# Kernel optimization log

Hardware: AMD Instinct MI355X
Metric: run time of the kernel (lower is better)

Reference implementation:

```python
import jax, jax.numpy as jnp
import numpy as np

FP8_MAX = 448.0  # e4m3 max
SCALE_MARGIN = 0.8


def _fp8_quant_dequant(t, scale):
    # scaled value is <= 448*0.8 by construction, so no saturation/overflow
    q = (t / scale).astype(jnp.float8_e4m3fn)
    return q.astype(jnp.float32) * scale


def setup_inputs() -> dict:
    key = jax.random.key(0)
    k1, k2 = jax.random.split(key)
    B, S, D_IN, D_OUT = 4, 2048, 2048, 2048
    x = jax.random.normal(k1, (B, S, D_IN), dtype=jnp.float32)
    weight = jax.random.normal(k2, (D_OUT, D_IN), dtype=jnp.float32)
    bias = jnp.zeros((D_OUT,), dtype=jnp.float32)
    return {"x": x, "weight": weight, "bias": bias}


def reference(x, weight, bias):
    # Shared FP8ScalingManager: amax history = [amax_x] for x, then [amax_x, amax_w] for w.
    amax_x = jnp.max(jnp.abs(x))
    amax_w = jnp.max(jnp.abs(weight))
    x_scale = amax_x / (FP8_MAX * SCALE_MARGIN)
    w_scale = jnp.maximum(amax_x, amax_w) / (FP8_MAX * SCALE_MARGIN)  # history max
    x_scale = jax.lax.stop_gradient(x_scale)  # .item() detaches in torch
    w_scale = jax.lax.stop_gradient(w_scale)
    # quantize to fp8 e4m3, dequantize, scaled matmul (math of torch._scaled_mm)
    x_dq = _fp8_quant_dequant(x, x_scale)      # [B,S,Din]
    w_dq = _fp8_quant_dequant(weight, w_scale)  # [Dout,Din]
    out = jnp.einsum('bsd,od->bso', x_dq, w_dq)  # [B,S,Dout]
    return out + bias
```

## Files before the change

### kernel.cpp

```cpp
#include <hip/hip_runtime.h>
#include <stdint.h>

typedef float v4f __attribute__((ext_vector_type(4)));
typedef int v8i __attribute__((ext_vector_type(8)));

#define FP8_DENOM 358.4f


__device__ __forceinline__ unsigned pack4_fp8(float a, float b, float c, float d) {
  int v = 0;
  v = __builtin_amdgcn_cvt_pk_fp8_f32(a, b, v, false);
  v = __builtin_amdgcn_cvt_pk_fp8_f32(c, d, v, true);
  return (unsigned)v;
}

__device__ __forceinline__ void gload_lds16(const void* g, void* l) {
  __builtin_amdgcn_global_load_lds(
      (const __attribute__((address_space(1))) uint32_t*)(uintptr_t)g,
      (__attribute__((address_space(3))) uint32_t*)(uint32_t)(uintptr_t)l,
      16, 0, 0);
}


__global__ void __launch_bounds__(256) amax_part(const float4* __restrict__ x,
                                                 const float4* __restrict__ w,
                                                 unsigned* __restrict__ amax) {
  const int b = blockIdx.x, t = threadIdx.x;
  const float4* p = (b < 1024) ? x : w;
  const long base = (long)((b < 1024) ? b : (b - 1024)) * 4096;
  float m0 = 0.f, m1 = 0.f, m2 = 0.f, m3 = 0.f;
#pragma unroll
  for (int j = 0; j < 4; ++j) {
    float4 v0 = p[base + (j * 4 + 0) * 256 + t];
    float4 v1 = p[base + (j * 4 + 1) * 256 + t];
    float4 v2 = p[base + (j * 4 + 2) * 256 + t];
    float4 v3 = p[base + (j * 4 + 3) * 256 + t];
    m0 = fmaxf(m0, fmaxf(fmaxf(fabsf(v0.x), fabsf(v0.y)), fmaxf(fabsf(v0.z), fabsf(v0.w))));
    m1 = fmaxf(m1, fmaxf(fmaxf(fabsf(v1.x), fabsf(v1.y)), fmaxf(fabsf(v1.z), fabsf(v1.w))));
    m2 = fmaxf(m2, fmaxf(fmaxf(fabsf(v2.x), fabsf(v2.y)), fmaxf(fabsf(v2.z), fabsf(v2.w))));
    m3 = fmaxf(m3, fmaxf(fmaxf(fabsf(v3.x), fabsf(v3.y)), fmaxf(fabsf(v3.z), fabsf(v3.w))));
  }
  float m = fmaxf(fmaxf(m0, m1), fmaxf(m2, m3));
#pragma unroll
  for (int off = 32; off > 0; off >>= 1)
    m = fmaxf(m, __shfl_down(m, off, 64));
  __shared__ float red[4];
  const int lane = t & 63, wvid = t >> 6;
  if (lane == 0) red[wvid] = m;
  __syncthreads();
  if (t == 0)
    atomicMax(amax + ((b < 1024) ? 0 : 1),
              __float_as_uint(fmaxf(fmaxf(red[0], red[1]), fmaxf(red[2], red[3]))));
}


__global__ void __launch_bounds__(256) quant2_kernel(
    const float4* __restrict__ x, unsigned* __restrict__ xq,
    const float4* __restrict__ w, unsigned* __restrict__ wq,
    const unsigned* __restrict__ amax) {
  const int t = threadIdx.x;
  const int isw = ((int)blockIdx.x >= 4096) ? 1 : 0;
  const float ax = __uint_as_float(amax[0]);
  const float aw = __uint_as_float(amax[1]);
  const float s = (isw ? fmaxf(ax, aw) : ax) / FP8_DENOM;
  const float rs = 1.0f / s;
  const float4* in = isw ? w : x;
  unsigned* outq = isw ? wq : xq;
  const long base = (long)(isw ? ((int)blockIdx.x - 4096) : (int)blockIdx.x) * 1024;
#pragma unroll
  for (int j = 0; j < 4; ++j) {
    float4 v = in[base + j * 256 + t];
    outq[base + j * 256 + t] = pack4_fp8(v.x * rs, v.y * rs, v.z * rs, v.w * rs);
  }
}


__global__ void __launch_bounds__(512, 2) gemm_mx(
    const uint8_t* __restrict__ Aq, const uint8_t* __restrict__ Bq,
    const float* __restrict__ bias, float* __restrict__ out,
    const unsigned* __restrict__ amax) {
  constexpr int K = 2048, N = 2048, BK = 128, ITERS = K / BK;
  __shared__ alignas(16) uint8_t sA[2][256 * BK];
  __shared__ alignas(16) uint8_t sB[2][256 * BK];

  const int tid = threadIdx.x;
  const int lane = tid & 63;
  const int wid = tid >> 6;
  const int wy = wid >> 2, wx = wid & 3;
  const long tileM = (long)blockIdx.y * 256;
  const long tileN = (long)blockIdx.x * 256;

  v4f acc[8][4];
#pragma unroll
  for (int i = 0; i < 8; ++i)
#pragma unroll
    for (int j = 0; j < 4; ++j) acc[i][j] = (v4f)(0.f);

  const int srow = tid >> 3;
  const int schunk = (tid & 7) ^ (srow & 7);
  const uint8_t* gA = Aq + (tileM + srow) * K + schunk * 16;
  const uint8_t* gB = Bq + (tileN + srow) * K + schunk * 16;

  const int q = lane >> 4;
  const int mrow = lane & 15;
  const int sw = mrow & 7;
  const int aoff0 = (wy * 128 + mrow) * BK + 16 * ((2 * q) ^ sw);
  const int aoff1 = (wy * 128 + mrow) * BK + 16 * ((2 * q + 1) ^ sw);
  const int boff0 = (wx * 64 + mrow) * BK + 16 * ((2 * q) ^ sw);
  const int boff1 = (wx * 64 + mrow) * BK + 16 * ((2 * q + 1) ^ sw);

  auto stage = [&](int buf, int k0) {
#pragma unroll
    for (int s = 0; s < 4; ++s) {
      gload_lds16(gA + (long)s * 64 * K + k0, &sA[buf][s * 8192 + tid * 16]);
      gload_lds16(gB + (long)s * 64 * K + k0, &sB[buf][s * 8192 + tid * 16]);
    }
  };

  stage(0, 0);
  for (int it = 0; it < ITERS; ++it) {
    __syncthreads();
    if (it + 1 < ITERS) stage((it + 1) & 1, (it + 1) * BK);

    const uint8_t* bufA = sA[it & 1];
    const uint8_t* bufB = sB[it & 1];
    union Frag { v8i v; uint4 h[2]; };
    Frag b[4];
#pragma unroll
    for (int j = 0; j < 4; ++j) {
      b[j].h[0] = *(const uint4*)(bufB + boff0 + j * 16 * BK);
      b[j].h[1] = *(const uint4*)(bufB + boff1 + j * 16 * BK);
    }
    __builtin_amdgcn_s_setprio(1);
#pragma unroll
    for (int i = 0; i < 8; ++i) {
      Frag a;
      a.h[0] = *(const uint4*)(bufA + aoff0 + i * 16 * BK);
      a.h[1] = *(const uint4*)(bufA + aoff1 + i * 16 * BK);
#pragma unroll
      for (int j = 0; j < 4; ++j)
        acc[i][j] = __builtin_amdgcn_mfma_scale_f32_16x16x128_f8f6f4(
            a.v, b[j].v, acc[i][j],  0,  0,
             0, 0x7F7F7F7F,  0, 0x7F7F7F7F);
    }
    __builtin_amdgcn_s_setprio(0);
  }

  const float ax = __uint_as_float(amax[0]);
  const float aw = __uint_as_float(amax[1]);
  const float scale = (ax / FP8_DENOM) * (fmaxf(ax, aw) / FP8_DENOM);
#pragma unroll
  for (int j = 0; j < 4; ++j) {
    const long col = tileN + wx * 64 + j * 16 + mrow;
    const float bv = bias[col];
#pragma unroll
    for (int i = 0; i < 8; ++i) {
      const long row = tileM + wy * 128 + i * 16 + q * 4;
#pragma unroll
      for (int r = 0; r < 4; ++r)
        out[(row + r) * N + col] = acc[i][j][r] * scale + bv;
    }
  }
}


extern "C" void kernel_launch(void* const* d_in, const int* in_sizes, int n_in,
                              void* d_out, int out_size, void* d_ws, size_t ws_size,
                              hipStream_t stream) {
  const float* x = (const float*)d_in[0];
  const float* w = (const float*)d_in[1];
  const float* bias = (const float*)d_in[2];
  float* out = (float*)d_out;

  const int M = 8192, N = 2048, K = 2048;
  const long nx = (long)M * K;

  unsigned* amax = (unsigned*)d_ws;
  uint8_t* xq = (uint8_t*)d_ws + 8192;
  uint8_t* wq = xq + nx;

  hipMemsetAsync(amax, 0, 8, stream);
  amax_part<<<1280, 256, 0, stream>>>((const float4*)x, (const float4*)w, amax);
  quant2_kernel<<<5120, 256, 0, stream>>>((const float4*)x, (unsigned*)xq,
                                          (const float4*)w, (unsigned*)wq, amax);
  gemm_mx<<<dim3(N / 256, M / 256), 512, 0, stream>>>(xq, wq, bias, out, amax);
}
```

Baseline: 177.7 us.

## Prefetch two K-tiles ahead in GEMM and split amax into smaller blocks

```diff
diff --git a/kernel.cpp b/kernel.cpp
--- a/kernel.cpp
+++ b/kernel.cpp
@@ -26,21 +26,17 @@
                                                  const float4* __restrict__ w,
                                                  unsigned* __restrict__ amax) {
   const int b = blockIdx.x, t = threadIdx.x;
-  const float4* p = (b < 1024) ? x : w;
-  const long base = (long)((b < 1024) ? b : (b - 1024)) * 4096;
-  float m0 = 0.f, m1 = 0.f, m2 = 0.f, m3 = 0.f;
+  const int isw = (b >= 2048) ? 1 : 0;
+  const float4* p = isw ? w : x;
+  const long base = (long)(isw ? (b - 2048) : b) * 2048;
+  float4 v[8];
 #pragma unroll
-  for (int j = 0; j < 4; ++j) {
-    float4 v0 = p[base + (j * 4 + 0) * 256 + t];
-    float4 v1 = p[base + (j * 4 + 1) * 256 + t];
-    float4 v2 = p[base + (j * 4 + 2) * 256 + t];
-    float4 v3 = p[base + (j * 4 + 3) * 256 + t];
-    m0 = fmaxf(m0, fmaxf(fmaxf(fabsf(v0.x), fabsf(v0.y)), fmaxf(fabsf(v0.z), fabsf(v0.w))));
-    m1 = fmaxf(m1, fmaxf(fmaxf(fabsf(v1.x), fabsf(v1.y)), fmaxf(fabsf(v1.z), fabsf(v1.w))));
-    m2 = fmaxf(m2, fmaxf(fmaxf(fabsf(v2.x), fabsf(v2.y)), fmaxf(fabsf(v2.z), fabsf(v2.w))));
-    m3 = fmaxf(m3, fmaxf(fmaxf(fabsf(v3.x), fabsf(v3.y)), fmaxf(fabsf(v3.z), fabsf(v3.w))));
-  }
-  float m = fmaxf(fmaxf(m0, m1), fmaxf(m2, m3));
+  for (int j = 0; j < 8; ++j) v[j] = p[base + j * 256 + t];
+  float m = 0.f;
+#pragma unroll
+  for (int j = 0; j < 8; ++j)
+    m = fmaxf(m, fmaxf(fmaxf(fabsf(v[j].x), fabsf(v[j].y)),
+                       fmaxf(fabsf(v[j].z), fabsf(v[j].w))));
 #pragma unroll
   for (int off = 32; off > 0; off >>= 1)
     m = fmaxf(m, __shfl_down(m, off, 64));
@@ -49,7 +45,7 @@
   if (lane == 0) red[wvid] = m;
   __syncthreads();
   if (t == 0)
-    atomicMax(amax + ((b < 1024) ? 0 : 1),
+    atomicMax(amax + isw,
               __float_as_uint(fmaxf(fmaxf(red[0], red[1]), fmaxf(red[2], red[3]))));
 }
 
@@ -118,9 +114,15 @@
   };
 
   stage(0, 0);
+  stage(1, BK);
+
   for (int it = 0; it < ITERS; ++it) {
-    __syncthreads();
-    if (it + 1 < ITERS) stage((it + 1) & 1, (it + 1) * BK);
+    if (it == ITERS - 1)
+      asm volatile("s_waitcnt vmcnt(0)" ::: "memory");
+    else
+      asm volatile("s_waitcnt vmcnt(8)" ::: "memory");
+    __builtin_amdgcn_s_barrier();
+    __builtin_amdgcn_sched_barrier(0);
 
     const uint8_t* bufA = sA[it & 1];
     const uint8_t* bufB = sB[it & 1];
@@ -144,6 +146,11 @@
              0, 0x7F7F7F7F,  0, 0x7F7F7F7F);
     }
     __builtin_amdgcn_s_setprio(0);
+
+    __builtin_amdgcn_sched_barrier(0);
+    asm volatile("s_waitcnt lgkmcnt(0)" ::: "memory");
+    __builtin_amdgcn_s_barrier();
+    if (it + 2 < ITERS) stage(it & 1, (it + 2) * BK);
   }
 
   const float ax = __uint_as_float(amax[0]);
@@ -180,7 +187,7 @@
   uint8_t* wq = xq + nx;
 
   hipMemsetAsync(amax, 0, 8, stream);
-  amax_part<<<1280, 256, 0, stream>>>((const float4*)x, (const float4*)w, amax);
+  amax_part<<<2560, 256, 0, stream>>>((const float4*)x, (const float4*)w, amax);
   quant2_kernel<<<5120, 256, 0, stream>>>((const float4*)x, (unsigned*)xq,
                                           (const float4*)w, (unsigned*)wq, amax);
   gemm_mx<<<dim3(N / 256, M / 256), 512, 0, stream>>>(xq, wq, bias, out, amax);
```

After: 193.2 us. +8.7%, slower.

## Split GEMM main loop into phased barriers with staggered A/B prefetch and XCD tile remap

Applied to the files above, without the earlier changes.

```diff
diff --git a/kernel.cpp b/kernel.cpp
--- a/kernel.cpp
+++ b/kernel.cpp
@@ -26,8 +26,9 @@
                                                  const float4* __restrict__ w,
                                                  unsigned* __restrict__ amax) {
   const int b = blockIdx.x, t = threadIdx.x;
-  const float4* p = (b < 1024) ? x : w;
-  const long base = (long)((b < 1024) ? b : (b - 1024)) * 4096;
+  const int isw = (b >= 1024) ? 1 : 0;
+  const float4* p = isw ? w : x;
+  const long base = (long)(isw ? (b - 1024) : b) * 4096;
   float m0 = 0.f, m1 = 0.f, m2 = 0.f, m3 = 0.f;
 #pragma unroll
   for (int j = 0; j < 4; ++j) {
@@ -49,7 +50,7 @@
   if (lane == 0) red[wvid] = m;
   __syncthreads();
   if (t == 0)
-    atomicMax(amax + ((b < 1024) ? 0 : 1),
+    atomicMax(amax + isw,
               __float_as_uint(fmaxf(fmaxf(red[0], red[1]), fmaxf(red[2], red[3]))));
 }
 
@@ -87,8 +88,11 @@
   const int lane = tid & 63;
   const int wid = tid >> 6;
   const int wy = wid >> 2, wx = wid & 3;
-  const long tileM = (long)blockIdx.y * 256;
-  const long tileN = (long)blockIdx.x * 256;
+
+  const int orig = (int)blockIdx.y * (int)gridDim.x + (int)blockIdx.x;
+  const int wg = (orig & 7) * 32 + (orig >> 3);
+  const long tileM = (long)(wg >> 3) * 256;
+  const long tileN = (long)(wg & 7) * 256;
 
   v4f acc[8][4];
 #pragma unroll
@@ -109,41 +113,69 @@
   const int boff0 = (wx * 64 + mrow) * BK + 16 * ((2 * q) ^ sw);
   const int boff1 = (wx * 64 + mrow) * BK + 16 * ((2 * q + 1) ^ sw);
 
-  auto stage = [&](int buf, int k0) {
-#pragma unroll
-    for (int s = 0; s < 4; ++s) {
+  auto stageA = [&](int buf, int k0) {
+#pragma unroll
+    for (int s = 0; s < 4; ++s)
       gload_lds16(gA + (long)s * 64 * K + k0, &sA[buf][s * 8192 + tid * 16]);
+  };
+  auto stageB = [&](int buf, int k0) {
+#pragma unroll
+    for (int s = 0; s < 4; ++s)
       gload_lds16(gB + (long)s * 64 * K + k0, &sB[buf][s * 8192 + tid * 16]);
+  };
+
+  stageA(0, 0);
+  stageB(0, 0);
+
+  union Frag { v8i v; uint4 h[2]; };
+
+  for (int it = 0; it < ITERS; ++it) {
+    const int cur = it & 1;
+    const uint8_t* bufA = sA[cur];
+    const uint8_t* bufB = sB[cur];
+    const bool pf = (it + 1 < ITERS);
+
+    Frag b[4];
+#pragma unroll
+    for (int p = 0; p < 4; ++p) {
+      if (p == 0) {
+        if (pf) {
+          stageA(cur ^ 1, (it + 1) * BK);
+          asm volatile("s_waitcnt vmcnt(4)" ::: "memory");
+        } else {
+          asm volatile("s_waitcnt vmcnt(0)" ::: "memory");
+        }
+        __builtin_amdgcn_s_barrier();
+        __builtin_amdgcn_sched_barrier(0);
+#pragma unroll
+        for (int j = 0; j < 4; ++j) {
+          b[j].h[0] = *(const uint4*)(bufB + boff0 + j * 16 * BK);
+          b[j].h[1] = *(const uint4*)(bufB + boff1 + j * 16 * BK);
+        }
+      }
+      if (p == 1 && pf) stageB(cur ^ 1, (it + 1) * BK);
+
+      Frag a0, a1;
+      a0.h[0] = *(const uint4*)(bufA + aoff0 + (2 * p + 0) * 16 * BK);
+      a0.h[1] = *(const uint4*)(bufA + aoff1 + (2 * p + 0) * 16 * BK);
+      a1.h[0] = *(const uint4*)(bufA + aoff0 + (2 * p + 1) * 16 * BK);
+      a1.h[1] = *(const uint4*)(bufA + aoff1 + (2 * p + 1) * 16 * BK);
+
+      asm volatile("s_waitcnt lgkmcnt(0)" ::: "memory");
+      __builtin_amdgcn_sched_barrier(0);
+      __builtin_amdgcn_s_setprio(1);
+#pragma unroll
+      for (int j = 0; j < 4; ++j)
+        acc[2 * p + 0][j] = __builtin_amdgcn_mfma_scale_f32_16x16x128_f8f6f4(
+            a0.v, b[j].v, acc[2 * p + 0][j], 0, 0, 0, 0x7F7F7F7F, 0, 0x7F7F7F7F);
+#pragma unroll
+      for (int j = 0; j < 4; ++j)
+        acc[2 * p + 1][j] = __builtin_amdgcn_mfma_scale_f32_16x16x128_f8f6f4(
+            a1.v, b[j].v, acc[2 * p + 1][j], 0, 0, 0, 0x7F7F7F7F, 0, 0x7F7F7F7F);
+      __builtin_amdgcn_s_setprio(0);
+      __builtin_amdgcn_sched_barrier(0);
+      __builtin_amdgcn_s_barrier();
     }
-  };
-
-  stage(0, 0);
-  for (int it = 0; it < ITERS; ++it) {
-    __syncthreads();
-    if (it + 1 < ITERS) stage((it + 1) & 1, (it + 1) * BK);
-
-    const uint8_t* bufA = sA[it & 1];
-    const uint8_t* bufB = sB[it & 1];
-    union Frag { v8i v; uint4 h[2]; };
-    Frag b[4];
-#pragma unroll
-    for (int j = 0; j < 4; ++j) {
-      b[j].h[0] = *(const uint4*)(bufB + boff0 + j * 16 * BK);
-      b[j].h[1] = *(const uint4*)(bufB + boff1 + j * 16 * BK);
-    }
-    __builtin_amdgcn_s_setprio(1);
-#pragma unroll
-    for (int i = 0; i < 8; ++i) {
-      Frag a;
-      a.h[0] = *(const uint4*)(bufA + aoff0 + i * 16 * BK);
-      a.h[1] = *(const uint4*)(bufA + aoff1 + i * 16 * BK);
-#pragma unroll
-      for (int j = 0; j < 4; ++j)
-        acc[i][j] = __builtin_amdgcn_mfma_scale_f32_16x16x128_f8f6f4(
-            a.v, b[j].v, acc[i][j],  0,  0,
-             0, 0x7F7F7F7F,  0, 0x7F7F7F7F);
-    }
-    __builtin_amdgcn_s_setprio(0);
   }
 
   const float ax = __uint_as_float(amax[0]);
```

Result: no change. 178.7 us (+0.5%).

## Deepen GEMM prefetch pipeline with manual waitcnt barriers and swizzle tile order

Applied to the files above, without the earlier changes.

```diff
diff --git a/kernel.cpp b/kernel.cpp
--- a/kernel.cpp
+++ b/kernel.cpp
@@ -26,8 +26,9 @@
                                                  const float4* __restrict__ w,
                                                  unsigned* __restrict__ amax) {
   const int b = blockIdx.x, t = threadIdx.x;
-  const float4* p = (b < 1024) ? x : w;
-  const long base = (long)((b < 1024) ? b : (b - 1024)) * 4096;
+  const int isw = (b >= 1024) ? 1 : 0;
+  const float4* p = isw ? w : x;
+  const long base = (long)(isw ? (b - 1024) : b) * 4096;
   float m0 = 0.f, m1 = 0.f, m2 = 0.f, m3 = 0.f;
 #pragma unroll
   for (int j = 0; j < 4; ++j) {
@@ -49,7 +50,7 @@
   if (lane == 0) red[wvid] = m;
   __syncthreads();
   if (t == 0)
-    atomicMax(amax + ((b < 1024) ? 0 : 1),
+    atomicMax(amax + isw,
               __float_as_uint(fmaxf(fmaxf(red[0], red[1]), fmaxf(red[2], red[3]))));
 }
 
@@ -87,8 +88,11 @@
   const int lane = tid & 63;
   const int wid = tid >> 6;
   const int wy = wid >> 2, wx = wid & 3;
-  const long tileM = (long)blockIdx.y * 256;
-  const long tileN = (long)blockIdx.x * 256;
+
+  const int orig = (int)blockIdx.y * (int)gridDim.x + (int)blockIdx.x;
+  const int wg = (orig & 7) * 32 + (orig >> 3);
+  const long tileM = (long)(wg >> 3) * 256;
+  const long tileN = (long)(wg & 7) * 256;
 
   v4f acc[8][4];
 #pragma unroll
@@ -118,32 +122,50 @@
   };
 
   stage(0, 0);
+  stage(1, BK);
+
+  union Frag { v8i v; uint4 h[2]; };
+
   for (int it = 0; it < ITERS; ++it) {
-    __syncthreads();
-    if (it + 1 < ITERS) stage((it + 1) & 1, (it + 1) * BK);
-
-    const uint8_t* bufA = sA[it & 1];
-    const uint8_t* bufB = sB[it & 1];
-    union Frag { v8i v; uint4 h[2]; };
-    Frag b[4];
+    const int cur = it & 1;
+
+    if (it + 1 < ITERS)
+      asm volatile("s_waitcnt vmcnt(8)" ::: "memory");
+    else
+      asm volatile("s_waitcnt vmcnt(0)" ::: "memory");
+    __builtin_amdgcn_s_barrier();
+    __builtin_amdgcn_sched_barrier(0);
+
+    const uint8_t* bufA = sA[cur];
+    const uint8_t* bufB = sB[cur];
+
+    Frag a[8], b[4];
 #pragma unroll
     for (int j = 0; j < 4; ++j) {
       b[j].h[0] = *(const uint4*)(bufB + boff0 + j * 16 * BK);
       b[j].h[1] = *(const uint4*)(bufB + boff1 + j * 16 * BK);
     }
+#pragma unroll
+    for (int i = 0; i < 8; ++i) {
+      a[i].h[0] = *(const uint4*)(bufA + aoff0 + i * 16 * BK);
+      a[i].h[1] = *(const uint4*)(bufA + aoff1 + i * 16 * BK);
+    }
+
     __builtin_amdgcn_s_setprio(1);
 #pragma unroll
-    for (int i = 0; i < 8; ++i) {
-      Frag a;
-      a.h[0] = *(const uint4*)(bufA + aoff0 + i * 16 * BK);
-      a.h[1] = *(const uint4*)(bufA + aoff1 + i * 16 * BK);
+    for (int i = 0; i < 8; ++i)
 #pragma unroll
       for (int j = 0; j < 4; ++j)
         acc[i][j] = __builtin_amdgcn_mfma_scale_f32_16x16x128_f8f6f4(
-            a.v, b[j].v, acc[i][j],  0,  0,
+            a[i].v, b[j].v, acc[i][j],  0,  0,
              0, 0x7F7F7F7F,  0, 0x7F7F7F7F);
-    }
     __builtin_amdgcn_s_setprio(0);
+
+    if (it + 2 < ITERS) {
+      asm volatile("s_waitcnt lgkmcnt(0)" ::: "memory");
+      __builtin_amdgcn_s_barrier();
+      stage(cur, (it + 2) * BK);
+    }
   }
 
   const float ax = __uint_as_float(amax[0]);
```

New measurement: 179.4 us. Within noise of the previous version (+0.9%).
